# Optimization experiments

Measured on AMD Instinct MI355X. Metric: run time of the kernel, lower is better.

## Reference

```python
import jax, jax.numpy as jnp
import numpy as np

B, S, T, H, E = 256, 512, 16, 1024, 512  # batch, src_len, trg_steps, hidden, emb_dim


def setup_inputs() -> dict:
    key = jax.random.key(0)
    ks = jax.random.split(key, 10)
    rn = lambda k, sh: jax.random.normal(k, sh, dtype=jnp.float32) * 0.05
    return {
        "trg_emb": rn(ks[0], (B, T, E)),
        "h0": rn(ks[1], (B, H)),
        "c0": rn(ks[2], (B, H)),
        "ctx": rn(ks[3], (B, S, H)),
        "src_len": jax.random.randint(ks[4], (B,), 1, S + 1, dtype=jnp.int32),
        "W_ih": rn(ks[5], (4 * H, E + H)),  # input-feeding: lstm in = emb + hidden
        "W_hh": rn(ks[6], (4 * H, H)),
        "b_ih": jnp.zeros((4 * H,), jnp.float32),
        "b_hh": jnp.zeros((4 * H,), jnp.float32),
        "W_in": rn(ks[7], (H, H)),    # attention linear_in (no bias)
        "W_out": rn(ks[8], (H, 2 * H)),  # attention linear_out (no bias)
    }


def reference(trg_emb, h0, c0, ctx, src_len, W_ih, W_hh, b_ih, b_hh, W_in, W_out):
    # mask[b, s] = s < src_len[b]
    mask = jnp.arange(S)[None, :] < src_len[:, None]  # (B, S)
    neg = jnp.float32(-1e9)

    def step(carry, emb_t):
        h, c, h_tilde = carry  # each (B, H); emb_t (B, E)
        # input feeding: concat target embedding with previous attentional vector
        x = jnp.concatenate([emb_t, h_tilde], axis=1)  # (B, E+H)
        gates = x @ W_ih.T + b_ih + h @ W_hh.T + b_hh  # (B, 4H), pytorch gate order i,f,g,o
        i, f, g, o = jnp.split(gates, 4, axis=1)
        i = jax.nn.sigmoid(i); f = jax.nn.sigmoid(f)
        g = jnp.tanh(g);       o = jax.nn.sigmoid(o)
        c = f * c + i * g
        h = o * jnp.tanh(c)
        # Luong soft-dot attention with src_len masking
        target = h @ W_in.T                                # (B, H)
        scores = jnp.einsum('bsh,bh->bs', ctx, target)     # (B, S)
        scores = jnp.where(mask, scores, neg)
        attn = jax.nn.softmax(scores, axis=-1)
        weighted = jnp.einsum('bs,bsh->bh', attn, ctx)     # (B, H)
        h_tilde = jnp.tanh(jnp.concatenate([weighted, h], axis=1) @ W_out.T)
        return (h, c, h_tilde), h_tilde

    # initial h_tilde = init_hidden[0] (per the original code)
    (h_f, c_f, _), hs = jax.lax.scan(step, (h0, c0, h0), jnp.swapaxes(trg_emb, 0, 1))
    output = jnp.swapaxes(hs, 0, 1)  # (B, T, H)
    return output, h_f, c_f
```

## Files before the change

kernel.cpp:

```cpp
#include <hip/hip_runtime.h>
#include <cstdint>
#include <cstddef>


#define B_ 256
#define S_ 512
#define T_ 16
#define H_ 1024
#define E_ 512
#define NBUF 4

typedef unsigned short u16;
using short8 = __attribute__((ext_vector_type(8))) short;
using f32x4  = __attribute__((ext_vector_type(4))) float;

__device__ __forceinline__ float bf2f(u16 u) {
  union { uint32_t i; float f; } v; v.i = ((uint32_t)u) << 16; return v.f;
}
__device__ __forceinline__ u16 f2bf(float f) {
  union { uint32_t i; float f; } v; v.f = f;
  uint32_t r = v.i + 0x7fffu + ((v.i >> 16) & 1u);
  return (u16)(r >> 16);
}
__device__ __forceinline__ ushort4 cvt4bf(float4 v) {
  ushort4 o; o.x = f2bf(v.x); o.y = f2bf(v.y); o.z = f2bf(v.z); o.w = f2bf(v.w);
  return o;
}
__device__ __forceinline__ float sigmoidf_(float x) { return 1.f / (1.f + __expf(-x)); }

__device__ __forceinline__ void gload_lds16(const void* g, void* l) {
  __builtin_amdgcn_global_load_lds(
      (const __attribute__((address_space(1))) void*)g,
      (__attribute__((address_space(3))) void*)l, 16, 0, 0);
}

struct Reg3 { const u16* A; int lda; const u16* B; int ldb; int kt; };

template <int EPI>
__global__ __launch_bounds__(128) void gemm_k(Reg3 r0, Reg3 r1, Reg3 r2,
                                              int nmb,
                                              float* __restrict__ Cf,
                                              u16* __restrict__ Cb,
                                              const float* __restrict__ bsum,
                                              float* __restrict__ cst,
                                              float* __restrict__ h32o,
                                              u16* __restrict__ hbfo,
                                              const int tstep) {
  __shared__ u16 smA[NBUF][64 * 64];
  __shared__ u16 smB[NBUF][64 * 64];
  const int tid = threadIdx.x;
  const int lane = tid & 63;
  const int wave = tid >> 6;
  const int m0 = (blockIdx.x % nmb) * 64;
  const int n0 = (blockIdx.x / nmb) * 64;
  const int row16 = lane & 15;
  const int kg = lane >> 4;
  const int nt = r0.kt + r1.kt + r2.kt;

  auto stage = [&](int ti, int buf) {
    const int k01 = r0.kt + r1.kt;
    const u16* Ap = (ti < r0.kt) ? r0.A : (ti < k01) ? r1.A : r2.A;
    const u16* Bp = (ti < r0.kt) ? r0.B : (ti < k01) ? r1.B : r2.B;
    const int lda = (ti < r0.kt) ? r0.lda : (ti < k01) ? r1.lda : r2.lda;
    const int ldb = (ti < r0.kt) ? r0.ldb : (ti < k01) ? r1.ldb : r2.ldb;
    const int base = (ti < r0.kt) ? 0 : (ti < k01) ? r0.kt : k01;
    const int kr = (ti - base) << 6;
#pragma unroll
    for (int j = 0; j < 4; ++j) {
      const int c = j * 128 + tid;
      const int row = c >> 3, q = c & 7;
      gload_lds16(Ap + (size_t)(m0 + row) * lda + kr + ((q ^ (row & 7)) << 3),
                  (char*)&smA[buf][0] + (size_t)(j * 128 + wave * 64) * 16);
    }
#pragma unroll
    for (int j = 0; j < 4; ++j) {
      const int c = j * 128 + tid;
      const int row = c >> 3, q = c & 7;
      gload_lds16(Bp + (size_t)(n0 + row) * ldb + kr + ((q ^ (row & 7)) << 3),
                  (char*)&smB[buf][0] + (size_t)(j * 128 + wave * 64) * 16);
    }
  };

  f32x4 acc[4][2] = {};
  stage(0, 0);
  if (nt > 1) stage(1, 1);
  for (int ti = 0; ti < nt; ++ti) {
    const int buf = ti & 3;
    if (ti + 2 < nt) {
      stage(ti + 2, (ti + 2) & 3);
      asm volatile("s_waitcnt vmcnt(16)" ::: "memory");
    } else if (ti + 1 < nt) {
      asm volatile("s_waitcnt vmcnt(8)" ::: "memory");
    } else {
      asm volatile("s_waitcnt vmcnt(0)" ::: "memory");
    }
    __builtin_amdgcn_s_barrier();
    __builtin_amdgcn_sched_barrier(0);
#pragma unroll
    for (int ks = 0; ks < 2; ++ks) {
      short8 af[4], bfr[2];
#pragma unroll
      for (int mi = 0; mi < 4; ++mi) {
        const int R = mi * 16 + row16;
        af[mi] = *(const short8*)((const char*)&smA[buf][0] +
                                  (size_t)(((R << 3) | ((ks * 4 + kg) ^ (R & 7))) << 4));
      }
#pragma unroll
      for (int ni = 0; ni < 2; ++ni) {
        const int R = wave * 32 + ni * 16 + row16;
        bfr[ni] = *(const short8*)((const char*)&smB[buf][0] +
                                   (size_t)(((R << 3) | ((ks * 4 + kg) ^ (R & 7))) << 4));
      }
      asm volatile("s_waitcnt lgkmcnt(0)" ::: "memory");
      __builtin_amdgcn_sched_barrier(0);
#pragma unroll
      for (int mi = 0; mi < 4; ++mi)
#pragma unroll
        for (int ni = 0; ni < 2; ++ni)
          acc[mi][ni] = __builtin_amdgcn_mfma_f32_16x16x32_bf16(af[mi], bfr[ni], acc[mi][ni], 0, 0, 0);
      __builtin_amdgcn_sched_barrier(0);
    }
  }
#pragma unroll
  for (int mi = 0; mi < 4; ++mi) {
#pragma unroll
    for (int ni = 0; ni < 2; ++ni) {
#pragma unroll
      for (int r = 0; r < 4; ++r) {
        const int row = m0 + mi * 16 + (kg << 2) + r;
        const int col = n0 + wave * 32 + ni * 16 + row16;
        float v = acc[mi][ni][r];
        if (EPI == 1) {
          Cb[row * H_ + col] = f2bf(v);
        } else if (EPI == 2) {
          float tv = tanhf(v);
          Cf[(size_t)row * (T_ * H_) + (size_t)tstep * H_ + col] = tv;
          Cb[row * H_ + col] = f2bf(tv);
        } else {
          v += bsum[col];
          float v1 = __shfl_xor(v, 1);
          float v2 = __shfl_xor(v, 2);
          float v3 = __shfl_xor(v, 3);
          if ((lane & 3) == 0) {
            const int u = col >> 2;
            float iv = sigmoidf_(v);
            float fv = sigmoidf_(v1);
            float gv = tanhf(v2);
            float ov = sigmoidf_(v3);
            float cn = fv * cst[row * H_ + u] + iv * gv;
            float hn = ov * tanhf(cn);
            cst[row * H_ + u] = cn;
            h32o[row * H_ + u] = hn;
            hbfo[row * H_ + u] = f2bf(hn);
          }
        }
      }
    }
  }
}

__device__ __forceinline__ int fidx(int lane, int j) {
  return (j << 6) + ((lane + (j << 2)) & 63);
}

__global__ __launch_bounds__(1024) void attn_k(const u16* __restrict__ tgt,
                                               const u16* __restrict__ ctxc,
                                               const int* __restrict__ offs,
                                               const int* __restrict__ src_len,
                                               u16* __restrict__ wwbf) {
  __shared__ float facc[8][1024];
  __shared__ float fm[16], fl[16];
  const int b = blockIdx.x;
  const int tid = threadIdx.x;
  const int lane = tid & 63;
  const int wave = tid >> 6;
  const int len = src_len[b];
  const u16* cb = ctxc + ((size_t)offs[b] << 10);

  float tg[16];
  {
    const u16* tp = tgt + b * H_ + lane * 16;
    short8 v1 = *(const short8*)tp;
    short8 v2 = *(const short8*)(tp + 8);
#pragma unroll
    for (int j = 0; j < 8; ++j) { tg[j] = bf2f((u16)v1[j]); tg[8 + j] = bf2f((u16)v2[j]); }
  }

  float m = -1e30f, l = 0.f;
  float acc[16];
#pragma unroll
  for (int j = 0; j < 16; ++j) acc[j] = 0.f;

  for (int s = wave; s < len; s += 16) {
    const u16* cr = cb + ((size_t)s << 10) + (lane << 4);
    short8 v1 = *(const short8*)cr;
    short8 v2 = *(const short8*)(cr + 8);
    float cf[16];
#pragma unroll
    for (int j = 0; j < 8; ++j) { cf[j] = bf2f((u16)v1[j]); cf[8 + j] = bf2f((u16)v2[j]); }
    float x = 0.f;
#pragma unroll
    for (int j = 0; j < 16; ++j) x += cf[j] * tg[j];
#pragma unroll
    for (int off = 1; off < 64; off <<= 1) x += __shfl_xor(x, off);
    if (x > m) {
      float sc_ = __expf(m - x);
      l *= sc_;
#pragma unroll
      for (int j = 0; j < 16; ++j) acc[j] *= sc_;
      m = x;
    }
    float p = __expf(x - m);
    l += p;
#pragma unroll
    for (int j = 0; j < 16; ++j) acc[j] += p * cf[j];
  }

  if (wave >= 8) {
#pragma unroll
    for (int j = 0; j < 16; ++j) facc[wave - 8][fidx(lane, j)] = acc[j];
    if (lane == 0) { fm[wave] = m; fl[wave] = l; }
  }
  __syncthreads();
  if (wave < 8) {
    float pm = fm[8 + wave];
    float pl = fl[8 + wave];
    float M = fmaxf(m, pm);
    float e1 = __expf(m - M);
    float e2 = __expf(pm - M);
#pragma unroll
    for (int j = 0; j < 16; ++j) {
      float pv = facc[wave][fidx(lane, j)];
      facc[wave][fidx(lane, j)] = acc[j] * e1 + pv * e2;
    }
    if (lane == 0) { fm[wave] = M; fl[wave] = l * e1 + pl * e2; }
  }
  __syncthreads();
  float mstar = -1e30f;
#pragma unroll
  for (int w = 0; w < 8; ++w) mstar = fmaxf(mstar, fm[w]);
  float lsum = 0.f, asum = 0.f;
  const int ri = fidx(tid >> 4, tid & 15);
#pragma unroll
  for (int w = 0; w < 8; ++w) {
    float e = __expf(fm[w] - mstar);
    lsum += fl[w] * e;
    asum += facc[w][ri] * e;
  }
  wwbf[b * H_ + tid] = f2bf(asum / lsum);
}

__global__ __launch_bounds__(256) void scan_k(const int* __restrict__ len,
                                              int* __restrict__ offs) {
  __shared__ int tmp[256];
  const int tid = threadIdx.x;
  const int v = len[tid];
  tmp[tid] = v;
  __syncthreads();
  for (int off = 1; off < 256; off <<= 1) {
    int t = (tid >= off) ? tmp[tid - off] : 0;
    __syncthreads();
    tmp[tid] += t;
    __syncthreads();
  }
  offs[tid] = tmp[tid] - v;
}

__global__ __launch_bounds__(256) void ctx_compact(const float* __restrict__ ctx,
                                                   const int* __restrict__ src_len,
                                                   const int* __restrict__ offs,
                                                   u16* __restrict__ ctxc) {
  const int b = blockIdx.x;
  const int n4 = src_len[b] << 8;
  const float4* s = (const float4*)(ctx + ((size_t)b << 19));
  ushort4* d = (ushort4*)(ctxc + ((size_t)offs[b] << 10));
  for (int i = threadIdx.x; i < n4; i += 256) d[i] = cvt4bf(s[i]);
}

__global__ __launch_bounds__(256) void convert_all(
    const float* __restrict__ W_ih, const float* __restrict__ W_hh,
    const float* __restrict__ W_in, const float* __restrict__ W_out,
    const float* __restrict__ trg_emb,
    const float* __restrict__ b_ih, const float* __restrict__ b_hh,
    const float* __restrict__ h0, const float* __restrict__ c0,
    u16* __restrict__ wWih, u16* __restrict__ wWhh, u16* __restrict__ wWin,
    u16* __restrict__ wWout, u16* __restrict__ wemb,
    float* __restrict__ wbsum, u16* __restrict__ wh0, u16* __restrict__ whtbf,
    float* __restrict__ wc) {
  const int gtid = blockIdx.x * 256 + threadIdx.x;
  const int GSZ = 1024 * 256;
  for (int i = gtid; i < 1572864; i += GSZ) {
    const int r = i / 384, c4 = i - r * 384;
    const int rp = ((r & 1023) << 2) + (r >> 10);
    ((ushort4*)wWih)[(size_t)rp * 384 + c4] = cvt4bf(((const float4*)W_ih)[i]);
  }
  for (int i = gtid; i < 1048576; i += GSZ) {
    const int r = i >> 8, c4 = i & 255;
    const int rp = ((r & 1023) << 2) + (r >> 10);
    ((ushort4*)wWhh)[(size_t)rp * 256 + c4] = cvt4bf(((const float4*)W_hh)[i]);
  }
  for (int i = gtid; i < 262144; i += GSZ)
    ((ushort4*)wWin)[i] = cvt4bf(((const float4*)W_in)[i]);
  for (int i = gtid; i < 524288; i += GSZ)
    ((ushort4*)wWout)[i] = cvt4bf(((const float4*)W_out)[i]);
  for (int i = gtid; i < 524288; i += GSZ)
    ((ushort4*)wemb)[i] = cvt4bf(((const float4*)trg_emb)[i]);
  if (gtid < 4096) {
    const int cp = ((gtid & 1023) << 2) + (gtid >> 10);
    wbsum[cp] = b_ih[gtid] + b_hh[gtid];
  }
  for (int i = gtid; i < 262144; i += GSZ) {
    u16 hb = f2bf(h0[i]);
    wh0[i] = hb;
    whtbf[i] = hb;
    wc[i] = c0[i];
  }
}

extern "C" void kernel_launch(void* const* d_in, const int* in_sizes, int n_in,
                              void* d_out, int out_size, void* d_ws, size_t ws_size,
                              hipStream_t stream) {
  const float* trg_emb = (const float*)d_in[0];
  const float* h0      = (const float*)d_in[1];
  const float* c0      = (const float*)d_in[2];
  const float* ctx     = (const float*)d_in[3];
  const int*   src_len = (const int*)d_in[4];
  const float* W_ih    = (const float*)d_in[5];
  const float* W_hh    = (const float*)d_in[6];
  const float* b_ih    = (const float*)d_in[7];
  const float* b_hh    = (const float*)d_in[8];
  const float* W_in    = (const float*)d_in[9];
  const float* W_out   = (const float*)d_in[10];
  float* out = (float*)d_out;

  char* w = (char*)d_ws;
  size_t off = 0;
  auto alloc = [&](size_t bytes) { char* p = w + off; off += bytes; return p; };
  u16*   wWih  = (u16*)  alloc(12582912);
  u16*   wWhh  = (u16*)  alloc(8388608);
  u16*   wWin  = (u16*)  alloc(2097152);
  u16*   wWout = (u16*)  alloc(4194304);
  u16*   wemb  = (u16*)  alloc(4194304);
  float* wbsum = (float*)alloc(16384);
  float* wh32  = (float*)alloc(1048576);
  float* wc    = (float*)alloc(1048576);
  u16*   wh0   = (u16*)  alloc(524288);
  u16*   wh1   = (u16*)  alloc(524288);
  u16*   whtbf = (u16*)  alloc(524288);
  u16*   wtgt  = (u16*)  alloc(524288);
  u16*   wwbf  = (u16*)  alloc(524288);
  int*   woffs = (int*)  alloc(1024);
  u16*   wctxc = (u16*)  alloc(268435456);
  (void)ws_size;

  scan_k<<<dim3(1), dim3(256), 0, stream>>>(src_len, woffs);
  convert_all<<<dim3(1024), dim3(256), 0, stream>>>(
      W_ih, W_hh, W_in, W_out, trg_emb, b_ih, b_hh, h0, c0,
      wWih, wWhh, wWin, wWout, wemb, wbsum, wh0, whtbf, wc);
  ctx_compact<<<dim3(B_), dim3(256), 0, stream>>>(ctx, src_len, woffs, wctxc);

  Reg3 rz = { nullptr, 0, nullptr, 0, 0 };
  for (int t = 0; t < T_; ++t) {
    const u16* hcur = (t & 1) ? wh1 : wh0;
    u16* hnxt = (t & 1) ? wh0 : wh1;
    Reg3 g0 = { wemb + (size_t)t * E_, T_ * E_, wWih,      E_ + H_, 8 };
    Reg3 g1 = { whtbf,                 H_,      wWih + E_, E_ + H_, 16 };
    Reg3 g2 = { hcur,                  H_,      wWhh,      H_,      16 };
    gemm_k<3><<<dim3(256), dim3(128), 0, stream>>>(
        g0, g1, g2, 4, nullptr, nullptr, wbsum, wc, wh32, hnxt, 0);
    Reg3 i0 = { hnxt, H_, wWin, H_, 16 };
    gemm_k<1><<<dim3(64), dim3(128), 0, stream>>>(
        i0, rz, rz, 4, nullptr, wtgt, nullptr, nullptr, nullptr, nullptr, 0);
    attn_k<<<dim3(B_), dim3(1024), 0, stream>>>(wtgt, wctxc, woffs, src_len, wwbf);
    Reg3 o0 = { wwbf, H_, wWout,      2 * H_, 16 };
    Reg3 o1 = { hnxt, H_, wWout + H_, 2 * H_, 16 };
    gemm_k<2><<<dim3(64), dim3(128), 0, stream>>>(
        o0, o1, rz, 4, out, whtbf, nullptr, nullptr, nullptr, nullptr, t);
  }
  hipMemcpyAsync(out + (size_t)B_ * T_ * H_, wh32, (size_t)B_ * H_ * sizeof(float),
                 hipMemcpyDeviceToDevice, stream);
  hipMemcpyAsync(out + (size_t)B_ * T_ * H_ + B_ * H_, wc, (size_t)B_ * H_ * sizeof(float),
                 hipMemcpyDeviceToDevice, stream);
}
```

Baseline: 2.096 ms.

## Fuse per-step GEMMs and attention into one kernel with flag-based sync

Each of the 16 timesteps previously ran four kernel launches: the gate GEMM, the target GEMM, attention and the output GEMM. These are replaced by a single 256-block kernel whose blocks pass work between stages through release/acquire flags in global memory, so only the rows a stage depends on must be ready. This cuts launch and drain overhead and allows partial overlap between stages. In exchange, the GEMM tiles move to four waves with 2x2 warp tiling, attention runs with 4 waves per batch row instead of 16, and the design depends on all 256 blocks being co-resident to avoid deadlock. The separate scan kernel is folded into ctx_compact, and the final h/c are written directly instead of copied afterwards.

```diff
diff --git a/kernel.cpp b/kernel.cpp
--- a/kernel.cpp
+++ b/kernel.cpp
@@ -34,25 +34,40 @@
       (__attribute__((address_space(3))) void*)l, 16, 0, 0);
 }
 
+__device__ __forceinline__ void st_flag(int* p) {
+  __hip_atomic_store(p, 1, __ATOMIC_RELEASE, __HIP_MEMORY_SCOPE_AGENT);
+}
+__device__ __forceinline__ void wait_flags(int* f, int nf, int tid) {
+  if (tid < nf) {
+    unsigned cnt = 0;
+    while (__hip_atomic_load(f + tid, __ATOMIC_RELAXED, __HIP_MEMORY_SCOPE_AGENT) == 0 &&
+           cnt < (1u << 18)) {
+      __builtin_amdgcn_s_sleep(2);
+      ++cnt;
+    }
+    int v = __hip_atomic_load(f + tid, __ATOMIC_ACQUIRE, __HIP_MEMORY_SCOPE_AGENT);
+    asm volatile("" :: "v"(v) : "memory");
+  }
+  __syncthreads();
+}
+
 struct Reg3 { const u16* A; int lda; const u16* B; int ldb; int kt; };
 
+union SMem {
+  struct { u16 A[NBUF][4096]; u16 B[NBUF][4096]; } g;
+  struct { float facc[2][1024]; float fm[4], fl[4]; } a;
+};
+
 template <int EPI>
-__global__ __launch_bounds__(128) void gemm_k(Reg3 r0, Reg3 r1, Reg3 r2,
-                                              int nmb,
-                                              float* __restrict__ Cf,
-                                              u16* __restrict__ Cb,
-                                              const float* __restrict__ bsum,
-                                              float* __restrict__ cst,
-                                              float* __restrict__ h32o,
-                                              u16* __restrict__ hbfo,
-                                              const int tstep) {
-  __shared__ u16 smA[NBUF][64 * 64];
-  __shared__ u16 smB[NBUF][64 * 64];
-  const int tid = threadIdx.x;
+__device__ void gemm4(SMem* sm, const int tid, const int m0, const int n0,
+                      const Reg3 r0, const Reg3 r1, const Reg3 r2,
+                      float* __restrict__ Cf, u16* __restrict__ Cb,
+                      const float* __restrict__ bsum, float* __restrict__ cst,
+                      u16* __restrict__ hbfo, float* __restrict__ outHC,
+                      const int tstep) {
   const int lane = tid & 63;
   const int wave = tid >> 6;
-  const int m0 = (blockIdx.x % nmb) * 64;
-  const int n0 = (blockIdx.x / nmb) * 64;
+  const int wm = wave >> 1, wn = wave & 1;
   const int row16 = lane & 15;
   const int kg = lane >> 4;
   const int nt = r0.kt + r1.kt + r2.kt;
@@ -66,31 +81,31 @@
     const int base = (ti < r0.kt) ? 0 : (ti < k01) ? r0.kt : k01;
     const int kr = (ti - base) << 6;
 #pragma unroll
-    for (int j = 0; j < 4; ++j) {
-      const int c = j * 128 + tid;
+    for (int j = 0; j < 2; ++j) {
+      const int c = j * 256 + tid;
       const int row = c >> 3, q = c & 7;
       gload_lds16(Ap + (size_t)(m0 + row) * lda + kr + ((q ^ (row & 7)) << 3),
-                  (char*)&smA[buf][0] + (size_t)(j * 128 + wave * 64) * 16);
-    }
-#pragma unroll
-    for (int j = 0; j < 4; ++j) {
-      const int c = j * 128 + tid;
+                  (char*)&sm->g.A[buf][0] + (size_t)(j * 256 + wave * 64) * 16);
+    }
+#pragma unroll
+    for (int j = 0; j < 2; ++j) {
+      const int c = j * 256 + tid;
       const int row = c >> 3, q = c & 7;
       gload_lds16(Bp + (size_t)(n0 + row) * ldb + kr + ((q ^ (row & 7)) << 3),
-                  (char*)&smB[buf][0] + (size_t)(j * 128 + wave * 64) * 16);
+                  (char*)&sm->g.B[buf][0] + (size_t)(j * 256 + wave * 64) * 16);
     }
   };
 
-  f32x4 acc[4][2] = {};
+  f32x4 acc[2][2] = {};
   stage(0, 0);
   if (nt > 1) stage(1, 1);
   for (int ti = 0; ti < nt; ++ti) {
     const int buf = ti & 3;
     if (ti + 2 < nt) {
       stage(ti + 2, (ti + 2) & 3);
-      asm volatile("s_waitcnt vmcnt(16)" ::: "memory");
+      asm volatile("s_waitcnt vmcnt(8)" ::: "memory");
     } else if (ti + 1 < nt) {
-      asm volatile("s_waitcnt vmcnt(8)" ::: "memory");
+      asm volatile("s_waitcnt vmcnt(4)" ::: "memory");
     } else {
       asm volatile("s_waitcnt vmcnt(0)" ::: "memory");
     }
@@ -98,37 +113,38 @@
     __builtin_amdgcn_sched_barrier(0);
 #pragma unroll
     for (int ks = 0; ks < 2; ++ks) {
-      short8 af[4], bfr[2];
-#pragma unroll
-      for (int mi = 0; mi < 4; ++mi) {
-        const int R = mi * 16 + row16;
-        af[mi] = *(const short8*)((const char*)&smA[buf][0] +
+      short8 af[2], bfr[2];
+#pragma unroll
+      for (int mi = 0; mi < 2; ++mi) {
+        const int R = wm * 32 + mi * 16 + row16;
+        af[mi] = *(const short8*)((const char*)&sm->g.A[buf][0] +
                                   (size_t)(((R << 3) | ((ks * 4 + kg) ^ (R & 7))) << 4));
       }
 #pragma unroll
       for (int ni = 0; ni < 2; ++ni) {
-        const int R = wave * 32 + ni * 16 + row16;
-        bfr[ni] = *(const short8*)((const char*)&smB[buf][0] +
+        const int R = wn * 32 + ni * 16 + row16;
+        bfr[ni] = *(const short8*)((const char*)&sm->g.B[buf][0] +
                                    (size_t)(((R << 3) | ((ks * 4 + kg) ^ (R & 7))) << 4));
       }
       asm volatile("s_waitcnt lgkmcnt(0)" ::: "memory");
       __builtin_amdgcn_sched_barrier(0);
 #pragma unroll
-      for (int mi = 0; mi < 4; ++mi)
+      for (int mi = 0; mi < 2; ++mi)
 #pragma unroll
         for (int ni = 0; ni < 2; ++ni)
           acc[mi][ni] = __builtin_amdgcn_mfma_f32_16x16x32_bf16(af[mi], bfr[ni], acc[mi][ni], 0, 0, 0);
       __builtin_amdgcn_sched_barrier(0);
     }
   }
-#pragma unroll
-  for (int mi = 0; mi < 4; ++mi) {
+  __builtin_amdgcn_s_barrier();
+#pragma unroll
+  for (int mi = 0; mi < 2; ++mi) {
 #pragma unroll
     for (int ni = 0; ni < 2; ++ni) {
 #pragma unroll
       for (int r = 0; r < 4; ++r) {
-        const int row = m0 + mi * 16 + (kg << 2) + r;
-        const int col = n0 + wave * 32 + ni * 16 + row16;
+        const int row = m0 + wm * 32 + mi * 16 + (kg << 2) + r;
+        const int col = n0 + wn * 32 + ni * 16 + row16;
         float v = acc[mi][ni][r];
         if (EPI == 1) {
           Cb[row * H_ + col] = f2bf(v);
@@ -150,8 +166,11 @@
             float cn = fv * cst[row * H_ + u] + iv * gv;
             float hn = ov * tanhf(cn);
             cst[row * H_ + u] = cn;
-            h32o[row * H_ + u] = hn;
             hbfo[row * H_ + u] = f2bf(hn);
+            if (outHC) {
+              outHC[row * H_ + u] = hn;
+              outHC[B_ * H_ + row * H_ + u] = cn;
+            }
           }
         }
       }
@@ -163,35 +182,29 @@
   return (j << 6) + ((lane + (j << 2)) & 63);
 }
 
-__global__ __launch_bounds__(1024) void attn_k(const u16* __restrict__ tgt,
-                                               const u16* __restrict__ ctxc,
-                                               const int* __restrict__ offs,
-                                               const int* __restrict__ src_len,
-                                               u16* __restrict__ wwbf) {
-  __shared__ float facc[8][1024];
-  __shared__ float fm[16], fl[16];
-  const int b = blockIdx.x;
-  const int tid = threadIdx.x;
+__device__ void attn4(SMem* sm, const int bid, const int tid,
+                      const u16* __restrict__ tgt, const u16* __restrict__ ctxc,
+                      const int* __restrict__ woffs, const int* __restrict__ src_len,
+                      u16* __restrict__ wwbf) {
   const int lane = tid & 63;
   const int wave = tid >> 6;
-  const int len = src_len[b];
-  const u16* cb = ctxc + ((size_t)offs[b] << 10);
+  const int len = src_len[bid];
+  const u16* cb = ctxc + ((size_t)woffs[bid] << 10);
 
   float tg[16];
   {
-    const u16* tp = tgt + b * H_ + lane * 16;
+    const u16* tp = tgt + bid * H_ + lane * 16;
     short8 v1 = *(const short8*)tp;
     short8 v2 = *(const short8*)(tp + 8);
 #pragma unroll
     for (int j = 0; j < 8; ++j) { tg[j] = bf2f((u16)v1[j]); tg[8 + j] = bf2f((u16)v2[j]); }
   }
-
   float m = -1e30f, l = 0.f;
   float acc[16];
 #pragma unroll
   for (int j = 0; j < 16; ++j) acc[j] = 0.f;
 
-  for (int s = wave; s < len; s += 16) {
+  for (int s = wave; s < len; s += 4) {
     const u16* cr = cb + ((size_t)s << 10) + (lane << 4);
     short8 v1 = *(const short8*)cr;
     short8 v2 = *(const short8*)(cr + 8);
@@ -216,65 +229,112 @@
     for (int j = 0; j < 16; ++j) acc[j] += p * cf[j];
   }
 
-  if (wave >= 8) {
-#pragma unroll
-    for (int j = 0; j < 16; ++j) facc[wave - 8][fidx(lane, j)] = acc[j];
-    if (lane == 0) { fm[wave] = m; fl[wave] = l; }
+  if (wave >= 2) {
+#pragma unroll
+    for (int j = 0; j < 16; ++j) sm->a.facc[wave - 2][fidx(lane, j)] = acc[j];
+    if (lane == 0) { sm->a.fm[wave] = m; sm->a.fl[wave] = l; }
   }
   __syncthreads();
-  if (wave < 8) {
-    float pm = fm[8 + wave];
-    float pl = fl[8 + wave];
+  if (wave < 2) {
+    float pm = sm->a.fm[wave + 2];
+    float pl = sm->a.fl[wave + 2];
     float M = fmaxf(m, pm);
     float e1 = __expf(m - M);
     float e2 = __expf(pm - M);
 #pragma unroll
     for (int j = 0; j < 16; ++j) {
-      float pv = facc[wave][fidx(lane, j)];
-      facc[wave][fidx(lane, j)] = acc[j] * e1 + pv * e2;
-    }
-    if (lane == 0) { fm[wave] = M; fl[wave] = l * e1 + pl * e2; }
+      float pv = sm->a.facc[wave][fidx(lane, j)];
+      sm->a.facc[wave][fidx(lane, j)] = acc[j] * e1 + pv * e2;
+    }
+    if (lane == 0) { sm->a.fm[wave] = M; sm->a.fl[wave] = l * e1 + pl * e2; }
   }
   __syncthreads();
-  float mstar = -1e30f;
-#pragma unroll
-  for (int w = 0; w < 8; ++w) mstar = fmaxf(mstar, fm[w]);
-  float lsum = 0.f, asum = 0.f;
-  const int ri = fidx(tid >> 4, tid & 15);
-#pragma unroll
-  for (int w = 0; w < 8; ++w) {
-    float e = __expf(fm[w] - mstar);
-    lsum += fl[w] * e;
-    asum += facc[w][ri] * e;
-  }
-  wwbf[b * H_ + tid] = f2bf(asum / lsum);
-}
-
-__global__ __launch_bounds__(256) void scan_k(const int* __restrict__ len,
-                                              int* __restrict__ offs) {
-  __shared__ int tmp[256];
+  const float m0v = sm->a.fm[0], m1v = sm->a.fm[1];
+  const float ms = fmaxf(m0v, m1v);
+  const float e0 = __expf(m0v - ms), e1 = __expf(m1v - ms);
+  const float inv = 1.f / (sm->a.fl[0] * e0 + sm->a.fl[1] * e1);
+  ushort4 o;
+#pragma unroll
+  for (int jj = 0; jj < 4; ++jj) {
+    const int c = tid * 4 + jj;
+    const int ri = fidx(c >> 4, c & 15);
+    float a = sm->a.facc[0][ri] * e0 + sm->a.facc[1][ri] * e1;
+    ((u16*)&o)[jj] = f2bf(a * inv);
+  }
+  *(ushort4*)(wwbf + bid * H_ + tid * 4) = o;
+}
+
+struct SP {
+  const u16 *wemb, *wWih, *wWhh, *wWin, *wWout;
+  const float* bsum;
+  float* wc;
+  const u16* hcur;
+  u16 *hnxt, *whtbf, *wtgt, *wwbf;
+  const u16* ctxc;
+  const int *woffs, *src_len;
+  float* out;
+  int *gflag, *tflag, *aflag;
+  int t;
+};
+
+__global__ __launch_bounds__(256) void step_k(SP P) {
+  __shared__ SMem sm;
   const int tid = threadIdx.x;
-  const int v = len[tid];
-  tmp[tid] = v;
+  const int bid = blockIdx.x;
+  const int m = bid & 3;
+  const int n = bid >> 2;
+  Reg3 rz = { nullptr, 0, nullptr, 0, 0 };
+
+  {
+    Reg3 g0 = { P.wemb + (size_t)P.t * E_, T_ * E_, P.wWih,      E_ + H_, 8 };
+    Reg3 g1 = { P.whtbf,                   H_,      P.wWih + E_, E_ + H_, 16 };
+    Reg3 g2 = { P.hcur,                    H_,      P.wWhh,      H_,      16 };
+    gemm4<3>(&sm, tid, m * 64, n * 64, g0, g1, g2, nullptr, nullptr,
+             P.bsum, P.wc, P.hnxt,
+             (P.t == T_ - 1) ? P.out + (size_t)B_ * T_ * H_ : nullptr, 0);
+    __syncthreads();
+    if (tid == 0) st_flag(P.gflag + m * 64 + n);
+  }
+  if (bid < 64) {
+    wait_flags(P.gflag + m * 64, 64, tid);
+    Reg3 i0 = { P.hnxt, H_, P.wWin, H_, 16 };
+    gemm4<1>(&sm, tid, m * 64, n * 64, i0, rz, rz, nullptr, P.wtgt,
+             nullptr, nullptr, nullptr, nullptr, 0);
+    __syncthreads();
+    if (tid == 0) st_flag(P.tflag + m * 16 + n);
+  }
+  wait_flags(P.tflag + (bid >> 6) * 16, 16, tid);
+  attn4(&sm, bid, tid, P.wtgt, P.ctxc, P.woffs, P.src_len, P.wwbf);
   __syncthreads();
-  for (int off = 1; off < 256; off <<= 1) {
-    int t = (tid >= off) ? tmp[tid - off] : 0;
-    __syncthreads();
-    tmp[tid] += t;
-    __syncthreads();
-  }
-  offs[tid] = tmp[tid] - v;
+  if (tid == 0) st_flag(P.aflag + (bid >> 6) * 64 + (bid & 63));
+  if (bid < 64) {
+    wait_flags(P.aflag + m * 64, 64, tid);
+    Reg3 o0 = { P.wwbf, H_, P.wWout,      2 * H_, 16 };
+    Reg3 o1 = { P.hnxt, H_, P.wWout + H_, 2 * H_, 16 };
+    gemm4<2>(&sm, tid, m * 64, n * 64, o0, o1, rz, P.out, P.whtbf,
+             nullptr, nullptr, nullptr, nullptr, P.t);
+  }
 }
 
 __global__ __launch_bounds__(256) void ctx_compact(const float* __restrict__ ctx,
                                                    const int* __restrict__ src_len,
-                                                   const int* __restrict__ offs,
+                                                   int* __restrict__ woffs,
                                                    u16* __restrict__ ctxc) {
+  __shared__ int tmp[256];
   const int b = blockIdx.x;
+  const int tid = threadIdx.x;
+  tmp[tid] = (tid < b) ? src_len[tid] : 0;
+  __syncthreads();
+  for (int o = 128; o > 0; o >>= 1) {
+    if (tid < o) tmp[tid] += tmp[tid + o];
+    __syncthreads();
+  }
+  const int off = tmp[0];
+  if (tid == 0) woffs[b] = off;
   const int n4 = src_len[b] << 8;
   const float4* s = (const float4*)(ctx + ((size_t)b << 19));
-  ushort4* d = (ushort4*)(ctxc + ((size_t)offs[b] << 10));
-  for (int i = threadIdx.x; i < n4; i += 256) d[i] = cvt4bf(s[i]);
+  ushort4* d = (ushort4*)(ctxc + ((size_t)off << 10));
+  for (int i = tid; i < n4; i += 256) d[i] = cvt4bf(s[i]);
 }
 
 __global__ __launch_bounds__(256) void convert_all(
@@ -342,7 +402,6 @@
   u16*   wWout = (u16*)  alloc(4194304);
   u16*   wemb  = (u16*)  alloc(4194304);
   float* wbsum = (float*)alloc(16384);
-  float* wh32  = (float*)alloc(1048576);
   float* wc    = (float*)alloc(1048576);
   u16*   wh0   = (u16*)  alloc(524288);
   u16*   wh1   = (u16*)  alloc(524288);
@@ -350,35 +409,32 @@
   u16*   wtgt  = (u16*)  alloc(524288);
   u16*   wwbf  = (u16*)  alloc(524288);
   int*   woffs = (int*)  alloc(1024);
+  int*   flags = (int*)  alloc(36864);
   u16*   wctxc = (u16*)  alloc(268435456);
   (void)ws_size;
-
-  scan_k<<<dim3(1), dim3(256), 0, stream>>>(src_len, woffs);
+  int* gflagA = flags;
+  int* tflagA = flags + 16 * 256;
+  int* aflagA = flags + 16 * 256 + 16 * 64;
+
+  hipMemsetAsync(flags, 0, 36864, stream);
   convert_all<<<dim3(1024), dim3(256), 0, stream>>>(
       W_ih, W_hh, W_in, W_out, trg_emb, b_ih, b_hh, h0, c0,
       wWih, wWhh, wWin, wWout, wemb, wbsum, wh0, whtbf, wc);
   ctx_compact<<<dim3(B_), dim3(256), 0, stream>>>(ctx, src_len, woffs, wctxc);
 
-  Reg3 rz = { nullptr, 0, nullptr, 0, 0 };
   for (int t = 0; t < T_; ++t) {
-    const u16* hcur = (t & 1) ? wh1 : wh0;
-    u16* hnxt = (t & 1) ? wh0 : wh1;
-    Reg3 g0 = { wemb + (size_t)t * E_, T_ * E_, wWih,      E_ + H_, 8 };
-    Reg3 g1 = { whtbf,                 H_,      wWih + E_, E_ + H_, 16 };
-    Reg3 g2 = { hcur,                  H_,      wWhh,      H_,      16 };
-    gemm_k<3><<<dim3(256), dim3(128), 0, stream>>>(
-        g0, g1, g2, 4, nullptr, nullptr, wbsum, wc, wh32, hnxt, 0);
-    Reg3 i0 = { hnxt, H_, wWin, H_, 16 };
-    gemm_k<1><<<dim3(64), dim3(128), 0, stream>>>(
-        i0, rz, rz, 4, nullptr, wtgt, nullptr, nullptr, nullptr, nullptr, 0);
-    attn_k<<<dim3(B_), dim3(1024), 0, stream>>>(wtgt, wctxc, woffs, src_len, wwbf);
-    Reg3 o0 = { wwbf, H_, wWout,      2 * H_, 16 };
-    Reg3 o1 = { hnxt, H_, wWout + H_, 2 * H_, 16 };
-    gemm_k<2><<<dim3(64), dim3(128), 0, stream>>>(
-        o0, o1, rz, 4, out, whtbf, nullptr, nullptr, nullptr, nullptr, t);
-  }
-  hipMemcpyAsync(out + (size_t)B_ * T_ * H_, wh32, (size_t)B_ * H_ * sizeof(float),
-                 hipMemcpyDeviceToDevice, stream);
-  hipMemcpyAsync(out + (size_t)B_ * T_ * H_ + B_ * H_, wc, (size_t)B_ * H_ * sizeof(float),
-                 hipMemcpyDeviceToDevice, stream);
-}
+    SP P;
+    P.wemb = wemb; P.wWih = wWih; P.wWhh = wWhh; P.wWin = wWin; P.wWout = wWout;
+    P.bsum = wbsum; P.wc = wc;
+    P.hcur = (t & 1) ? wh1 : wh0;
+    P.hnxt = (t & 1) ? wh0 : wh1;
+    P.whtbf = whtbf; P.wtgt = wtgt; P.wwbf = wwbf;
+    P.ctxc = wctxc; P.woffs = woffs; P.src_len = src_len;
+    P.out = out;
+    P.gflag = gflagA + t * 256;
+    P.tflag = tflagA + t * 64;
+    P.aflag = aflagA + t * 256;
+    P.t = t;
+    step_k<<<dim3(B_), dim3(256), 0, stream>>>(P);
+  }
+}
```

Result: slower. 2.935 ms (+40.0%).
